# Optimization experiments

Measured on AMD Instinct MI355X. Metric: run time of the kernel, lower is better.

Reference implementation:

```python
import jax, jax.numpy as jnp
import numpy as np

B, N, D, NH, DFF = 16, 512, 1024, 16, 4096
DK = D // NH


def _layer_norm(x, eps=1e-5):
    mu = jnp.mean(x, axis=-1, keepdims=True)
    var = jnp.var(x, axis=-1, keepdims=True)
    return (x - mu) * jax.lax.rsqrt(var + eps)


def setup_inputs() -> dict:
    key = jax.random.key(0)
    ks = jax.random.split(key, 12)
    s = 0.02
    return {
        "H": jax.random.normal(ks[0], (B, N, D), jnp.float32),
        "shortest_path_matrix": jax.random.normal(ks[1], (B, N, N), jnp.float32),
        "Wq": s * jax.random.normal(ks[2], (NH, D, DK), jnp.float32),
        "bq": jnp.zeros((NH, DK), jnp.float32),
        "Wk": s * jax.random.normal(ks[3], (NH, D, DK), jnp.float32),
        "bk": jnp.zeros((NH, DK), jnp.float32),
        "Wv": s * jax.random.normal(ks[4], (NH, D, DK), jnp.float32),
        "bv": jnp.zeros((NH, DK), jnp.float32),
        "Wo": s * jax.random.normal(ks[5], (D, D), jnp.float32),
        "bo": jnp.zeros((D,), jnp.float32),
        "W1": s * jax.random.normal(ks[6], (D, DFF), jnp.float32),
        "b1": jnp.zeros((DFF,), jnp.float32),
        "W2": s * jax.random.normal(ks[7], (DFF, D), jnp.float32),
        "b2": jnp.zeros((D,), jnp.float32),
    }


def reference(H, shortest_path_matrix, Wq, bq, Wk, bk, Wv, bv, Wo, bo, W1, b1, W2, b2):
    ln1 = _layer_norm(H)  # [B,N,D]
    # per-head projections: [B,H,N,DK]
    Q = jnp.einsum('bnd,hdk->bhnk', ln1, Wq) + bq[None, :, None, :]
    K = jnp.einsum('bnd,hdk->bhnk', ln1, Wk) + bk[None, :, None, :]
    V = jnp.einsum('bnd,hdk->bhnk', ln1, Wv) + bv[None, :, None, :]
    scale = 1.0 / jnp.sqrt(jnp.asarray(DK, Q.dtype))
    scores = jnp.einsum('bhnk,bhmk->bhnm', Q, K) * scale + shortest_path_matrix[:, None, :, :]
    A = jax.nn.softmax(scores, axis=-1)
    O = jnp.einsum('bhnm,bhmk->bhnk', A, V)  # [B,H,N,DK]
    O = jnp.transpose(O, (0, 2, 1, 3)).reshape(O.shape[0], O.shape[2], -1)  # [B,N,D]
    attn_out = O @ Wo + bo
    x = attn_out + H
    h = jax.nn.relu(_layer_norm(x) @ W1 + b1)
    return x + h @ W2 + b2
```

## Files before the change

kernel.cpp:

```cpp
#include <hip/hip_runtime.h>

#define BB   16
#define NN   512
#define DD   1024
#define NHH  16
#define DKK  64
#define DFF  4096
#define MM   (BB*NN)

typedef _Float16 h16;
typedef h16  h16x8 __attribute__((ext_vector_type(8)));
typedef h16  h16x4 __attribute__((ext_vector_type(4)));
typedef float f32x4 __attribute__((ext_vector_type(4)));

#define AS1 __attribute__((address_space(1)))
#define AS3 __attribute__((address_space(3)))

__device__ __forceinline__ void gld16(h16* lds_dst, const h16* g_src) {
  __builtin_amdgcn_global_load_lds((const AS1 void*)g_src, (AS3 void*)lds_dst, 16, 0, 0);
}

__global__ __launch_bounds__(256) void ln_k(const float* __restrict__ in, h16* __restrict__ out)
{
  const int row = blockIdx.x;
  const int tid = threadIdx.x;
  const float4 v = ((const float4*)(in + (long)row * DD))[tid];
  float s  = v.x + v.y + v.z + v.w;
  float ss = v.x*v.x + v.y*v.y + v.z*v.z + v.w*v.w;
#pragma unroll
  for (int d = 32; d > 0; d >>= 1) { s += __shfl_down(s, d); ss += __shfl_down(ss, d); }
  __shared__ float red[8];
  const int wv = tid >> 6, ln = tid & 63;
  if (ln == 0) { red[wv] = s; red[4 + wv] = ss; }
  __syncthreads();
  s  = red[0] + red[1] + red[2] + red[3];
  ss = red[4] + red[5] + red[6] + red[7];
  const float mean = s * (1.0f / DD);
  const float var  = ss * (1.0f / DD) - mean * mean;
  const float rstd = rsqrtf(var + 1e-5f);
  h16x4 o;
  o[0] = (h16)((v.x - mean) * rstd);
  o[1] = (h16)((v.y - mean) * rstd);
  o[2] = (h16)((v.z - mean) * rstd);
  o[3] = (h16)((v.w - mean) * rstd);
  ((h16x4*)(out + (long)row * DD))[tid] = o;
}

__global__ __launch_bounds__(256) void tcast_k(const float* __restrict__ src, h16* __restrict__ dst,
                                               int R, int C, long sB, long dB)
{
  __shared__ float tile[32][33];
  const float* s = src + (long)blockIdx.z * sB;
  h16* d = dst + (long)blockIdx.z * dB;
  const int c0 = blockIdx.x * 32, r0 = blockIdx.y * 32;
  const int tx = threadIdx.x & 31, ty = threadIdx.x >> 5;
#pragma unroll
  for (int i = 0; i < 32; i += 8)
    tile[ty + i][tx] = s[(long)(r0 + ty + i) * C + c0 + tx];
  __syncthreads();
#pragma unroll
  for (int i = 0; i < 32; i += 8)
    d[(long)(c0 + ty + i) * R + r0 + tx] = (h16)tile[tx][ty + i];
}

template<int EPI>
__global__ __launch_bounds__(256) void gemm_k(
    const h16* __restrict__ A, const h16* __restrict__ Bt, int K, int Nc,
    const float* __restrict__ bias0, const float* __restrict__ bias1,
    h16* __restrict__ o0, h16* __restrict__ o1,
    float* __restrict__ of, const float* __restrict__ addsrc)
{
  __shared__ h16 Asb[3 * 4096];
  __shared__ h16 Bsb[3 * 4096];
  const int tid  = threadIdx.x;
  const int wave = tid >> 6, lane = tid & 63;
  const int lr = lane & 15, lq = lane >> 4;

  const int nxw = gridDim.x, nyw = gridDim.y;
  const int orig = blockIdx.x + nxw * blockIdx.y;
  const int xcd = orig & 7, sseq = orig >> 3;
  const int by = xcd * (nyw >> 3) + sseq / nxw;
  const int bx = sseq % nxw;
  const int m0 = by * 128, n0 = bx * 128;
  const int wr = (wave >> 1) * 64, wc = (wave & 1) * 64;

  const int c0 = tid,       r0 = c0 >> 2, s0 = ((c0 & 3) ^ ((c0 >> 3) & 3)) * 8;
  const int c1 = tid + 256, r1 = c1 >> 2, s1 = ((c1 & 3) ^ ((c1 >> 3) & 3)) * 8;

  int offA[4], offB[4];
#pragma unroll
  for (int i = 0; i < 4; ++i) {
    const int ra = wr + i * 16 + lr;
    const int rb = wc + i * 16 + lr;
    offA[i] = ra * 32 + (lq ^ ((ra >> 1) & 3)) * 8;
    offB[i] = rb * 32 + (lq ^ ((rb >> 1) & 3)) * 8;
  }

  f32x4 acc[4][4] = {};

  auto STAGE = [&](int k0, int bi) {
    h16* Ad = Asb + bi * 4096;
    h16* Bd = Bsb + bi * 4096;
    gld16(Ad + c0 * 8, A  + (long)(m0 + r0) * K + k0 + s0);
    gld16(Ad + c1 * 8, A  + (long)(m0 + r1) * K + k0 + s1);
    gld16(Bd + c0 * 8, Bt + (long)(n0 + r0) * K + k0 + s0);
    gld16(Bd + c1 * 8, Bt + (long)(n0 + r1) * K + k0 + s1);
  };

  const int nt = K >> 5;
  STAGE(0, 0);
  STAGE(32, 1);
  int cur = 0;

  for (int t = 0; t < nt; ++t) {
    asm volatile("s_waitcnt lgkmcnt(0)" ::: "memory");
    if (t + 1 < nt) asm volatile("s_waitcnt vmcnt(4)" ::: "memory");
    else            asm volatile("s_waitcnt vmcnt(0)" ::: "memory");
    __builtin_amdgcn_sched_barrier(0);
    __builtin_amdgcn_s_barrier();
    asm volatile("" ::: "memory");

    if (t + 2 < nt) STAGE((t + 2) << 5, (cur + 2) % 3);

    const h16* Ac = Asb + cur * 4096;
    const h16* Bc = Bsb + cur * 4096;
    h16x8 af[4], bf[4];
#pragma unroll
    for (int i = 0; i < 4; ++i) {
      af[i] = *(const h16x8*)(Ac + offA[i]);
      bf[i] = *(const h16x8*)(Bc + offB[i]);
    }
    __builtin_amdgcn_s_setprio(1);
#pragma unroll
    for (int i = 0; i < 4; ++i)
#pragma unroll
      for (int j = 0; j < 4; ++j)
        acc[i][j] = __builtin_amdgcn_mfma_f32_16x16x32_f16(af[i], bf[j], acc[i][j], 0, 0, 0);
    __builtin_amdgcn_s_setprio(0);

    cur = (cur == 2) ? 0 : cur + 1;
  }

#pragma unroll
  for (int i = 0; i < 4; ++i) {
#pragma unroll
    for (int jn = 0; jn < 4; ++jn) {
#pragma unroll
      for (int j = 0; j < 4; ++j) {
        const int m   = m0 + wr + i * 16 + lq * 4 + j;
        const int col = n0 + wc + jn * 16 + lr;
        float v = acc[i][jn][j];
        if constexpr (EPI == 0) {
          const int w  = col >> 10;
          const int hh = (col >> 6) & 15, kk = col & 63;
          const int bidx = m >> 9, nq = m & 511;
          const int bcol = col & 1023;
          if (w == 0) o0[(((long)bidx * NHH + hh) * NN + nq) * DKK + kk] = (h16)(v + bias0[bcol]);
          else        o1[(((long)bidx * NHH + hh) * NN + nq) * DKK + kk] = (h16)(v + bias1[bcol]);
        } else if constexpr (EPI == 1) {
          of[(long)m * Nc + col] = v + bias0[col] + addsrc[(long)m * Nc + col];
        } else if constexpr (EPI == 2) {
          o0[(long)m * Nc + col] = (h16)fmaxf(v + bias0[col], 0.0f);
        } else if constexpr (EPI == 3) {
          of[(long)m * Nc + col] = v + bias0[col] + addsrc[(long)m * Nc + col];
        } else {
          const int bidx = col >> 9, nq = col & 511;
          o0[(((long)bidx * NHH + (m >> 6)) * DKK + (m & 63)) * NN + nq] = (h16)(v + bias0[m]);
        }
      }
    }
  }
}

__global__ __launch_bounds__(256) void attn_k(
    const h16* __restrict__ Qh, const h16* __restrict__ Kh, const h16* __restrict__ Vt,
    const float* __restrict__ spm, h16* __restrict__ Oh)
{
  __shared__ h16 Qs[128 * 64];
  __shared__ h16 Ks[2][64 * 64];
  __shared__ h16 Vts[2][64 * 64];
  __shared__ h16 Ps[4 * 32 * 64];
  const int tid  = threadIdx.x;
  const int wave = tid >> 6, lane = tid & 63;
  const int lr = lane & 15, lq = lane >> 4;
  const int b = blockIdx.z, h = blockIdx.y;
  const int q0 = blockIdx.x * 128;
  const long bh = (long)b * NHH + h;
  const h16* Qg = Qh + bh * NN * DKK;
  const h16* Kg = Kh + bh * NN * DKK;
  const h16* Vg = Vt + bh * DKK * NN;

#pragma unroll
  for (int r = 0; r < 4; ++r) {
    const int c = r * 256 + tid;
    const int row = c >> 3, sl = c & 7;
    gld16(Qs + c * 8, Qg + (long)(q0 + row) * DKK + ((sl ^ (row & 7)) * 8));
  }

  auto STAGEKV = [&](int kc, int bi) {
#pragma unroll
    for (int r = 0; r < 2; ++r) {
      const int c = r * 256 + tid;
      const int row = c >> 3, sl = c & 7;
      const int sg = (sl ^ (row & 7)) * 8;
      gld16(&Ks[bi][c * 8],  Kg + (long)(kc + row) * DKK + sg);
      gld16(&Vts[bi][c * 8], Vg + (long)row * NN + kc + sg);
    }
  };
  STAGEKV(0, 0);

  f32x4 acc[2][4] = {};
  float mrow[2][4], lsum[2][4];
#pragma unroll
  for (int a = 0; a < 2; ++a)
#pragma unroll
    for (int j = 0; j < 4; ++j) { mrow[a][j] = -3.0e38f; lsum[a][j] = 0.0f; }

  const int NT = NN / 64;
  for (int t = 0; t < NT; ++t) {
    const int kc = t * 64;
    asm volatile("s_waitcnt lgkmcnt(0)" ::: "memory");
    asm volatile("s_waitcnt vmcnt(0)" ::: "memory");
    __builtin_amdgcn_sched_barrier(0);
    __builtin_amdgcn_s_barrier();
    asm volatile("" ::: "memory");
    if (t + 1 < NT) STAGEKV(kc + 64, (t + 1) & 1);

    const h16* Kc = Ks[t & 1];
    const h16* Vc = Vts[t & 1];

    f32x4 s[2][4] = {};
#pragma unroll
    for (int ks = 0; ks < 2; ++ks) {
      h16x8 aq[2], bk4[4];
#pragma unroll
      for (int qm = 0; qm < 2; ++qm) {
        const int row = wave * 32 + qm * 16 + lr;
        aq[qm] = *(const h16x8*)(Qs + row * 64 + ((ks * 4 + lq) ^ (row & 7)) * 8);
      }
#pragma unroll
      for (int kn = 0; kn < 4; ++kn) {
        const int row = kn * 16 + lr;
        bk4[kn] = *(const h16x8*)(Kc + row * 64 + ((ks * 4 + lq) ^ (row & 7)) * 8);
      }
      __builtin_amdgcn_s_setprio(1);
#pragma unroll
      for (int qm = 0; qm < 2; ++qm)
#pragma unroll
        for (int kn = 0; kn < 4; ++kn)
          s[qm][kn] = __builtin_amdgcn_mfma_f32_16x16x32_f16(aq[qm], bk4[kn], s[qm][kn], 0, 0, 0);
      __builtin_amdgcn_s_setprio(0);
    }

    float pm[2][4];
#pragma unroll
    for (int qm = 0; qm < 2; ++qm)
#pragma unroll
      for (int j = 0; j < 4; ++j) pm[qm][j] = -3.0e38f;
#pragma unroll
    for (int qm = 0; qm < 2; ++qm)
#pragma unroll
      for (int kn = 0; kn < 4; ++kn)
#pragma unroll
        for (int j = 0; j < 4; ++j) {
          const int q = q0 + wave * 32 + qm * 16 + lq * 4 + j;
          const int key = kc + kn * 16 + lr;
          float v = s[qm][kn][j] * 0.125f + spm[((long)b * NN + q) * NN + key];
          s[qm][kn][j] = v;
          pm[qm][j] = fmaxf(pm[qm][j], v);
        }
#pragma unroll
    for (int qm = 0; qm < 2; ++qm)
#pragma unroll
      for (int j = 0; j < 4; ++j) {
#pragma unroll
        for (int d = 1; d < 16; d <<= 1) pm[qm][j] = fmaxf(pm[qm][j], __shfl_xor(pm[qm][j], d));
      }
    float corr[2][4];
#pragma unroll
    for (int qm = 0; qm < 2; ++qm)
#pragma unroll
      for (int j = 0; j < 4; ++j) {
        const float mn = fmaxf(mrow[qm][j], pm[qm][j]);
        corr[qm][j] = __expf(mrow[qm][j] - mn);
        mrow[qm][j] = mn;
        lsum[qm][j] *= corr[qm][j];
      }
    float rs[2][4] = {};
#pragma unroll
    for (int qm = 0; qm < 2; ++qm)
#pragma unroll
      for (int kn = 0; kn < 4; ++kn)
#pragma unroll
        for (int j = 0; j < 4; ++j) {
          const float pexp = __expf(s[qm][kn][j] - mrow[qm][j]);
          s[qm][kn][j] = pexp;
          rs[qm][j] += pexp;
        }
#pragma unroll
    for (int qm = 0; qm < 2; ++qm)
#pragma unroll
      for (int j = 0; j < 4; ++j) {
#pragma unroll
        for (int d = 1; d < 16; d <<= 1) rs[qm][j] += __shfl_xor(rs[qm][j], d);
        lsum[qm][j] += rs[qm][j];
      }
#pragma unroll
    for (int qm = 0; qm < 2; ++qm)
#pragma unroll
      for (int dn = 0; dn < 4; ++dn)
#pragma unroll
        for (int j = 0; j < 4; ++j) acc[qm][dn][j] *= corr[qm][j];

#pragma unroll
    for (int qm = 0; qm < 2; ++qm)
#pragma unroll
      for (int kn = 0; kn < 4; ++kn)
#pragma unroll
        for (int j = 0; j < 4; ++j) {
          const int row = qm * 16 + lq * 4 + j;
          const int sl  = (kn * 2 + (lr >> 3)) ^ (row & 7);
          Ps[wave * 2048 + row * 64 + sl * 8 + (lr & 7)] = (h16)s[qm][kn][j];
        }

#pragma unroll
    for (int ks = 0; ks < 2; ++ks) {
      h16x8 ap[2], bv4[4];
#pragma unroll
      for (int qm = 0; qm < 2; ++qm) {
        const int row = qm * 16 + lr;
        ap[qm] = *(const h16x8*)(Ps + wave * 2048 + row * 64 + ((ks * 4 + lq) ^ (row & 7)) * 8);
      }
#pragma unroll
      for (int dn = 0; dn < 4; ++dn) {
        const int row = dn * 16 + lr;
        bv4[dn] = *(const h16x8*)(Vc + row * 64 + ((ks * 4 + lq) ^ (row & 7)) * 8);
      }
      __builtin_amdgcn_s_setprio(1);
#pragma unroll
      for (int qm = 0; qm < 2; ++qm)
#pragma unroll
        for (int dn = 0; dn < 4; ++dn)
          acc[qm][dn] = __builtin_amdgcn_mfma_f32_16x16x32_f16(ap[qm], bv4[dn], acc[qm][dn], 0, 0, 0);
      __builtin_amdgcn_s_setprio(0);
    }
  }

  float rinv[2][4];
#pragma unroll
  for (int qm = 0; qm < 2; ++qm)
#pragma unroll
    for (int j = 0; j < 4; ++j) rinv[qm][j] = 1.0f / lsum[qm][j];
#pragma unroll
  for (int qm = 0; qm < 2; ++qm)
#pragma unroll
    for (int dn = 0; dn < 4; ++dn)
#pragma unroll
      for (int j = 0; j < 4; ++j) {
        const int q = q0 + wave * 32 + qm * 16 + lq * 4 + j;
        const int dk = dn * 16 + lr;
        Oh[((long)b * NN + q) * DD + h * DKK + dk] = (h16)(acc[qm][dn][j] * rinv[qm][j]);
      }
}

extern "C" void kernel_launch(void* const* d_in, const int* in_sizes, int n_in,
                              void* d_out, int out_size, void* d_ws, size_t ws_size,
                              hipStream_t stream)
{
  const float* H   = (const float*)d_in[0];
  const float* spm = (const float*)d_in[1];
  const float* Wq  = (const float*)d_in[2];
  const float* bq  = (const float*)d_in[3];
  const float* Wk  = (const float*)d_in[4];
  const float* bk  = (const float*)d_in[5];
  const float* Wv  = (const float*)d_in[6];
  const float* bv  = (const float*)d_in[7];
  const float* Wo  = (const float*)d_in[8];
  const float* bo  = (const float*)d_in[9];
  const float* W1  = (const float*)d_in[10];
  const float* b1  = (const float*)d_in[11];
  const float* W2  = (const float*)d_in[12];
  const float* b2  = (const float*)d_in[13];
  float* out = (float*)d_out;

  char* p = (char*)d_ws;
  auto alloc = [&](size_t bytes) { char* r = p; p += (bytes + 255) & ~(size_t)255; return r; };
  h16* ln1   = (h16*)alloc((size_t)MM * DD * 2);
  h16* wqkv  = (h16*)alloc((size_t)3 * DD * DD * 2);
  h16* wo_t  = (h16*)alloc((size_t)DD * DD * 2);
  h16* w1_t  = (h16*)alloc((size_t)DD * DFF * 2);
  h16* w2_t  = (h16*)alloc((size_t)DFF * DD * 2);
  h16* Qh    = (h16*)alloc((size_t)MM * DD * 2);
  h16* Kh    = (h16*)alloc((size_t)MM * DD * 2);
  h16* Vt    = (h16*)alloc((size_t)MM * DD * 2);
  h16* Oh    = (h16*)alloc((size_t)MM * DD * 2);
  float* x   = (float*)alloc((size_t)MM * DD * 4);
  h16* ln2 = ln1;
  h16* hff = Qh;

  ln_k<<<MM, 256, 0, stream>>>(H, ln1);
  tcast_k<<<dim3(2, 32, 16),  256, 0, stream>>>(Wq, wqkv,                 DD, DKK, (long)DD * DKK, (long)DKK * DD);
  tcast_k<<<dim3(2, 32, 16),  256, 0, stream>>>(Wk, wqkv + DD * DD,       DD, DKK, (long)DD * DKK, (long)DKK * DD);
  tcast_k<<<dim3(2, 32, 16),  256, 0, stream>>>(Wv, wqkv + 2 * DD * DD,   DD, DKK, (long)DD * DKK, (long)DKK * DD);
  tcast_k<<<dim3(32, 32, 1),  256, 0, stream>>>(Wo, wo_t, DD,  DD,  0, 0);
  tcast_k<<<dim3(128, 32, 1), 256, 0, stream>>>(W1, w1_t, DD,  DFF, 0, 0);
  tcast_k<<<dim3(32, 128, 1), 256, 0, stream>>>(W2, w2_t, DFF, DD,  0, 0);
  gemm_k<0><<<dim3(16, 64), 256, 0, stream>>>(ln1, wqkv, DD, 2 * DD, bq, bk, Qh, Kh, nullptr, nullptr);
  gemm_k<4><<<dim3(64, 8), 256, 0, stream>>>(wqkv + 2 * DD * DD, ln1, DD, MM, bv, nullptr, Vt, nullptr, nullptr, nullptr);
  attn_k<<<dim3(4, NHH, BB), 256, 0, stream>>>(Qh, Kh, Vt, spm, Oh);
  gemm_k<1><<<dim3(8, 64), 256, 0, stream>>>(Oh, wo_t, DD, DD, bo, nullptr, nullptr, nullptr, x, H);
  ln_k<<<MM, 256, 0, stream>>>(x, ln2);
  gemm_k<2><<<dim3(32, 64), 256, 0, stream>>>(ln2, w1_t, DD, DFF, b1, nullptr, hff, nullptr, nullptr, nullptr);
  gemm_k<3><<<dim3(8, 64), 256, 0, stream>>>(hff, w2_t, DFF, DD, b2, nullptr, nullptr, nullptr, out, x);
}
```

Before: 543.3 us.

## Split-K the Wo and W2 GEMMs with atomic accumulation into pre-initialised outputs

Adds a split-K mode to the GEMM: blockIdx.z selects a K slice and partial sums are atomically added into an fp32 output. A new elementwise kernel pre-fills that output with residual plus bias. The Wo GEMM is split in 2 and the W2 GEMM in 4, so the 512-tile launches become 1024 and 2048 blocks and fill the GPU better. In exchange it costs extra launches, an extra full read/write pass for initialisation, and many fp32 atomics to global memory, which also make the summation order nondeterministic.

```diff
diff --git a/kernel.cpp b/kernel.cpp
--- a/kernel.cpp
+++ b/kernel.cpp
@@ -63,9 +63,21 @@
     d[(long)(c0 + ty + i) * R + r0 + tx] = (h16)tile[tx][ty + i];
 }
 
+__global__ __launch_bounds__(256) void initadd_k(const float* __restrict__ add,
+                                                 const float* __restrict__ bias,
+                                                 float* __restrict__ out, int Nc4, long total4)
+{
+  for (long i = (long)blockIdx.x * 256 + threadIdx.x; i < total4; i += (long)gridDim.x * 256) {
+    const float4 a = ((const float4*)add)[i];
+    const float4 b = ((const float4*)bias)[i % Nc4];
+    float4 o; o.x = a.x + b.x; o.y = a.y + b.y; o.z = a.z + b.z; o.w = a.w + b.w;
+    ((float4*)out)[i] = o;
+  }
+}
+
 template<int EPI>
 __global__ __launch_bounds__(256) void gemm_k(
-    const h16* __restrict__ A, const h16* __restrict__ Bt, int K, int Nc,
+    const h16* __restrict__ A, const h16* __restrict__ Bt, int K, int ldk, int Nc,
     const float* __restrict__ bias0, const float* __restrict__ bias1,
     h16* __restrict__ o0, h16* __restrict__ o1,
     float* __restrict__ of, const float* __restrict__ addsrc)
@@ -75,6 +87,9 @@
   const int tid  = threadIdx.x;
   const int wave = tid >> 6, lane = tid & 63;
   const int lr = lane & 15, lq = lane >> 4;
+
+  A  += (long)blockIdx.z * K;
+  Bt += (long)blockIdx.z * K;
 
   const int nxw = gridDim.x, nyw = gridDim.y;
   const int orig = blockIdx.x + nxw * blockIdx.y;
@@ -101,10 +116,10 @@
   auto STAGE = [&](int k0, int bi) {
     h16* Ad = Asb + bi * 4096;
     h16* Bd = Bsb + bi * 4096;
-    gld16(Ad + c0 * 8, A  + (long)(m0 + r0) * K + k0 + s0);
-    gld16(Ad + c1 * 8, A  + (long)(m0 + r1) * K + k0 + s1);
-    gld16(Bd + c0 * 8, Bt + (long)(n0 + r0) * K + k0 + s0);
-    gld16(Bd + c1 * 8, Bt + (long)(n0 + r1) * K + k0 + s1);
+    gld16(Ad + c0 * 8, A  + (long)(m0 + r0) * ldk + k0 + s0);
+    gld16(Ad + c1 * 8, A  + (long)(m0 + r1) * ldk + k0 + s1);
+    gld16(Bd + c0 * 8, Bt + (long)(n0 + r0) * ldk + k0 + s0);
+    gld16(Bd + c1 * 8, Bt + (long)(n0 + r1) * ldk + k0 + s1);
   };
 
   const int nt = K >> 5;
@@ -163,9 +178,11 @@
           o0[(long)m * Nc + col] = (h16)fmaxf(v + bias0[col], 0.0f);
         } else if constexpr (EPI == 3) {
           of[(long)m * Nc + col] = v + bias0[col] + addsrc[(long)m * Nc + col];
-        } else {
+        } else if constexpr (EPI == 4) {
           const int bidx = col >> 9, nq = col & 511;
           o0[(((long)bidx * NHH + (m >> 6)) * DKK + (m & 63)) * NN + nq] = (h16)(v + bias0[m]);
+        } else {
+          atomicAdd(&of[(long)m * Nc + col], v);
         }
       }
     }
@@ -405,11 +422,13 @@
   tcast_k<<<dim3(32, 32, 1),  256, 0, stream>>>(Wo, wo_t, DD,  DD,  0, 0);
   tcast_k<<<dim3(128, 32, 1), 256, 0, stream>>>(W1, w1_t, DD,  DFF, 0, 0);
   tcast_k<<<dim3(32, 128, 1), 256, 0, stream>>>(W2, w2_t, DFF, DD,  0, 0);
-  gemm_k<0><<<dim3(16, 64), 256, 0, stream>>>(ln1, wqkv, DD, 2 * DD, bq, bk, Qh, Kh, nullptr, nullptr);
-  gemm_k<4><<<dim3(64, 8), 256, 0, stream>>>(wqkv + 2 * DD * DD, ln1, DD, MM, bv, nullptr, Vt, nullptr, nullptr, nullptr);
+  gemm_k<0><<<dim3(16, 64), 256, 0, stream>>>(ln1, wqkv, DD, DD, 2 * DD, bq, bk, Qh, Kh, nullptr, nullptr);
+  gemm_k<4><<<dim3(64, 8), 256, 0, stream>>>(wqkv + 2 * DD * DD, ln1, DD, DD, MM, bv, nullptr, Vt, nullptr, nullptr, nullptr);
   attn_k<<<dim3(4, NHH, BB), 256, 0, stream>>>(Qh, Kh, Vt, spm, Oh);
-  gemm_k<1><<<dim3(8, 64), 256, 0, stream>>>(Oh, wo_t, DD, DD, bo, nullptr, nullptr, nullptr, x, H);
+  initadd_k<<<2048, 256, 0, stream>>>(H, bo, x, DD / 4, (long)MM * DD / 4);
+  gemm_k<5><<<dim3(8, 64, 2), 256, 0, stream>>>(Oh, wo_t, DD / 2, DD, DD, nullptr, nullptr, nullptr, nullptr, x, nullptr);
   ln_k<<<MM, 256, 0, stream>>>(x, ln2);
-  gemm_k<2><<<dim3(32, 64), 256, 0, stream>>>(ln2, w1_t, DD, DFF, b1, nullptr, hff, nullptr, nullptr, nullptr);
-  gemm_k<3><<<dim3(8, 64), 256, 0, stream>>>(hff, w2_t, DFF, DD, b2, nullptr, nullptr, nullptr, out, x);
-}
+  gemm_k<2><<<dim3(32, 64), 256, 0, stream>>>(ln2, w1_t, DD, DD, DFF, b1, nullptr, hff, nullptr, nullptr, nullptr);
+  initadd_k<<<2048, 256, 0, stream>>>(x, b2, out, DD / 4, (long)MM * DD / 4);
+  gemm_k<5><<<dim3(8, 64, 4), 256, 0, stream>>>(hff, w2_t, DFF / 4, DFF, DD, nullptr, nullptr, nullptr, nullptr, out, nullptr);
+}
```

Result: slower. 646.0 us (+18.9%).
